# Kernel optimization log

Measured on AMD Instinct MI355X. Metric: run time of the kernel, lower is better.

Reference implementation:

```python
import jax, jax.numpy as jnp
import numpy as np

NUM_HEADS = 6
WS = 3

def setup_inputs() -> dict:
    key = jax.random.key(0)
    k1, k2, k3 = jax.random.split(key, 3)
    dim = 192
    x = jax.random.normal(k1, (2, dim, 48, 48, 48), dtype=jnp.float32)
    Wqkv = jax.random.normal(k2, (3 * dim, dim), dtype=jnp.float32) * (dim ** -0.5)
    Wproj = jax.random.normal(k3, (dim, dim), dtype=jnp.float32) * (dim ** -0.5)
    bproj = jnp.zeros((dim,), dtype=jnp.float32)
    return {"x": x, "Wqkv": Wqkv, "Wproj": Wproj, "bproj": bproj, "H": 384, "W": 288}

def reference(x, Wqkv, Wproj, bproj, H, W):
    b, c, h, w, d = x.shape
    xt = x.reshape(b, -1, c)                      # (B, N, C) with C = c, N = h*w*d
    B, N, C = xt.shape
    nh, ws = NUM_HEADS, WS
    hd = C // nh
    scale = hd ** -0.5
    hg, wg = H // ws, W // ws
    tg = hg * wg
    # window partition: (B, hg, ws, wg, ws, C) -> (B, hg, wg, ws, ws, C)
    xw = xt.reshape(B, hg, ws, wg, ws, C).transpose(0, 1, 3, 2, 4, 5)
    # fused QKV projection (no bias)
    qkv = jnp.einsum('bgvijc,oc->bgvijo', xw, Wqkv)          # (B,hg,wg,ws,ws,3C)
    qkv = qkv.reshape(B, tg, ws * ws, 3, nh, hd).transpose(3, 0, 1, 4, 2, 5)
    q, k, v = qkv[0], qkv[1], qkv[2]                          # (B, tg, nh, 9, hd)
    attn = jnp.einsum('bgnqd,bgnkd->bgnqk', q, k) * scale     # (B, tg, nh, 9, 9)
    attn = jax.nn.softmax(attn, axis=-1)
    out = jnp.einsum('bgnqk,bgnkd->bgnqd', attn, v)           # (B, tg, nh, 9, hd)
    out = out.transpose(0, 1, 3, 2, 4).reshape(B, hg, wg, ws, ws, C)
    out = jnp.swapaxes(out, 2, 3).reshape(B, N, C)            # un-window
    out = out @ Wproj.T + bproj
    return out.reshape(b, c, h, w, d)
```

## Files before the change

### kernel.cpp

```cpp
#include <hip/hip_runtime.h>

typedef _Float16 f16;
typedef _Float16 f16x4 __attribute__((ext_vector_type(4)));
typedef _Float16 f16x8 __attribute__((ext_vector_type(8)));
typedef float f32x4 __attribute__((ext_vector_type(4)));

#define TPB  576
#define NWIN 16
#define XS   200
#define WSS  200
#define QS   40
#define VS   264

#define WSQ_HALVES_PER_HEAD (96 * 200)
#define WSP_HALVES_PER_HEAD (192 * 40)
#define WS_NEEDED (230400 + 92160)

__device__ __forceinline__ void gload16(const void* g, void* l) {
    __builtin_amdgcn_global_load_lds(
        (const __attribute__((address_space(1))) unsigned int*)g,
        (__attribute__((address_space(3))) unsigned int*)l, 16, 0, 0);
}

__global__ __launch_bounds__(512) void conv_w(
    const float* __restrict__ Wqkv, const float* __restrict__ Wproj,
    f16* __restrict__ wsWq, f16* __restrict__ wsWp)
{
    int idx = blockIdx.x * 512 + threadIdx.x;
    if (idx < 110592) {
        int h = idx / (96 * 192), rem = idx % (96 * 192);
        int r = rem / 192, c = rem % 192;
        int grow = (r >> 5) * 192 + h * 32 + (r & 31);
        wsWq[(h * 96 + r) * 200 + c] = (f16)Wqkv[grow * 192 + c];
    } else {
        int j = idx - 110592;
        int h = j / (192 * 32), rem = j % (192 * 32);
        int r = rem / 32, c = rem % 32;
        wsWp[(h * 192 + r) * 40 + c] = (f16)Wproj[r * 192 + h * 32 + c];
    }
}

__global__ __launch_bounds__(TPB) void lsa_mfma10(
    const float* __restrict__ x, const f16* __restrict__ wsWq,
    const f16* __restrict__ wsWp, const float* __restrict__ bproj,
    float* __restrict__ out)
{
    __shared__ __attribute__((aligned(16))) f16 Xh[144 * XS];
    __shared__ __attribute__((aligned(16))) f16 Wh[96 * WSS];
    __shared__ __attribute__((aligned(16))) f16 Qh[144 * QS];
    __shared__ __attribute__((aligned(16))) f16 Kh[144 * QS];
    __shared__ __attribute__((aligned(16))) f16 Vt2[32 * VS];
    __shared__ __attribute__((aligned(16))) f16 AOh[144 * QS];
    __shared__ __attribute__((aligned(16))) f16 Wp[192 * QS];

    const int tid  = threadIdx.x;
    const int lane = tid & 63;
    const int w    = tid >> 6;
    const int ci   = w / 3;
    const int ti   = w % 3;
    const int l15  = lane & 15;
    const int lg   = lane >> 4;

    const int  bb    = blockIdx.x / 768;
    const int  gbase = (blockIdx.x % 768) * NWIN;
    const long rb0   = (long)bb * 110592 + (long)(gbase / 96) * 864 + (long)(gbase % 96) * 3;

    for (int l = tid; l < 2400; l += TPB)
        gload16(wsWq + l * 8, (char*)Wh + l * 16);
    for (int idx = tid; idx < 144 * 48; idx += TPB) {
        int t = idx / 48, c4 = idx % 48;
        int wi = t / 9, q = t - 9 * wi;
        long grow = rb0 + wi * 3 + (q / 3) * 288 + (q % 3);
        float4 xv = ((const float4*)x)[grow * 48 + c4];
        union { f16 h[4]; ushort4 u; } tmp;
        tmp.h[0] = (f16)xv.x; tmp.h[1] = (f16)xv.y; tmp.h[2] = (f16)xv.z; tmp.h[3] = (f16)xv.w;
        *(ushort4*)&Xh[t * XS + c4 * 4] = tmp.u;
    }
    {
        int4 z = {0, 0, 0, 0};
        for (int i2 = tid; i2 < (32 * VS * 2) / 16; i2 += TPB) ((int4*)Vt2)[i2] = z;
    }

    f32x4 pacc[3][4];
    #pragma unroll
    for (int a = 0; a < 3; ++a)
        #pragma unroll
        for (int bq = 0; bq < 4; ++bq)
            pacc[a][bq] = (f32x4){0.f, 0.f, 0.f, 0.f};

    __syncthreads();

    for (int h = 0; h < 6; ++h) {
        f32x4 qacc[2][3];
        #pragma unroll
        for (int c = 0; c < 2; ++c)
            #pragma unroll
            for (int t = 0; t < 3; ++t)
                qacc[c][t] = (f32x4){0.f, 0.f, 0.f, 0.f};
        #pragma unroll
        for (int kk = 0; kk < 6; ++kk) {
            f16x8 af[2], bf[3];
            #pragma unroll
            for (int c = 0; c < 2; ++c)
                af[c] = *(const f16x8*)&Wh[(16 * (ci + 3 * c) + l15) * WSS + kk * 32 + lg * 8];
            #pragma unroll
            for (int t = 0; t < 3; ++t)
                bf[t] = *(const f16x8*)&Xh[(16 * (ti + 3 * t) + l15) * XS + kk * 32 + lg * 8];
            #pragma unroll
            for (int c = 0; c < 2; ++c)
                #pragma unroll
                for (int t = 0; t < 3; ++t)
                    qacc[c][t] = __builtin_amdgcn_mfma_f32_16x16x32_f16(af[c], bf[t], qacc[c][t], 0, 0, 0);
        }
        #pragma unroll
        for (int c = 0; c < 2; ++c) {
            const int ct = ci + 3 * c;
            #pragma unroll
            for (int t = 0; t < 3; ++t) {
                const int token = 16 * (ti + 3 * t) + l15;
                f16x4 ph;
                ph[0] = (f16)qacc[c][t][0]; ph[1] = (f16)qacc[c][t][1];
                ph[2] = (f16)qacc[c][t][2]; ph[3] = (f16)qacc[c][t][3];
                if (ct < 2) {
                    *(f16x4*)&Qh[token * QS + ct * 16 + 4 * lg] = ph;
                } else if (ct < 4) {
                    *(f16x4*)&Kh[token * QS + (ct - 2) * 16 + 4 * lg] = ph;
                } else {
                    const int d0 = (ct - 4) * 16 + 4 * lg;
                    int wi = token / 9, qq = token - 9 * wi;
                    #pragma unroll
                    for (int r = 0; r < 4; ++r)
                        Vt2[(d0 + r) * VS + 16 * wi + qq] = ph[r];
                }
            }
        }
        __syncthreads();

        if (h < 5) {
            for (int l = tid; l < 2400; l += TPB)
                gload16(wsWq + (h + 1) * WSQ_HALVES_PER_HEAD + l * 8, (char*)Wh + l * 16);
        }
        for (int l = tid; l < 960; l += TPB)
            gload16(wsWp + h * WSP_HALVES_PER_HEAD + l * 8, (char*)Wp + l * 16);

        for (int wi = w; wi < NWIN; wi += 9) {
            int krow = 9 * wi + l15;
            krow = krow > 143 ? 143 : krow;
            f16x8 ak = *(const f16x8*)&Kh[krow * QS + lg * 8];
            f16x8 aq = *(const f16x8*)&Qh[krow * QS + lg * 8];
            f32x4 s = (f32x4){0.f, 0.f, 0.f, 0.f};
            s = __builtin_amdgcn_mfma_f32_16x16x32_f16(ak, aq, s, 0, 0, 0);
            float lgt[4];
            float mx = -1e30f;
            #pragma unroll
            for (int r = 0; r < 4; ++r) {
                int kx = 4 * lg + r;
                lgt[r] = (kx < 9) ? s[r] * 0.17677669529663687f : -1e30f;
                mx = fmaxf(mx, lgt[r]);
            }
            mx = fmaxf(mx, __shfl_xor(mx, 16));
            mx = fmaxf(mx, __shfl_xor(mx, 32));
            float e[4], sum = 0.f;
            #pragma unroll
            for (int r = 0; r < 4; ++r) {
                int kx = 4 * lg + r;
                e[r] = (kx < 9) ? __expf(lgt[r] - mx) : 0.f;
                sum += e[r];
            }
            sum += __shfl_xor(sum, 16);
            sum += __shfl_xor(sum, 32);
            float inv = 1.0f / sum;
            f16x4 p;
            p[0] = (f16)(e[0] * inv); p[1] = (f16)(e[1] * inv);
            p[2] = (f16)(e[2] * inv); p[3] = (f16)(e[3] * inv);
            #pragma unroll
            for (int dt = 0; dt < 2; ++dt) {
                f16x4 av = *(const f16x4*)&Vt2[(dt * 16 + l15) * VS + 16 * wi + 4 * lg];
                f32x4 o = (f32x4){0.f, 0.f, 0.f, 0.f};
                o = __builtin_amdgcn_mfma_f32_16x16x16f16(av, p, o, 0, 0, 0);
                if (l15 < 9) {
                    f16x4 oh;
                    oh[0] = (f16)o[0]; oh[1] = (f16)o[1]; oh[2] = (f16)o[2]; oh[3] = (f16)o[3];
                    *(f16x4*)&AOh[(9 * wi + l15) * QS + dt * 16 + 4 * lg] = oh;
                }
            }
        }
        __syncthreads();

        {
            f16x8 aof[3];
            #pragma unroll
            for (int a = 0; a < 3; ++a)
                aof[a] = *(const f16x8*)&AOh[(16 * (3 * ci + a) + l15) * QS + lg * 8];
            #pragma unroll
            for (int bq = 0; bq < 4; ++bq) {
                f16x8 bw = *(const f16x8*)&Wp[(16 * (4 * ti + bq) + l15) * QS + lg * 8];
                #pragma unroll
                for (int a = 0; a < 3; ++a)
                    pacc[a][bq] = __builtin_amdgcn_mfma_f32_16x16x32_f16(aof[a], bw, pacc[a][bq], 0, 0, 0);
            }
        }
    }

    float bv[4];
    #pragma unroll
    for (int bq = 0; bq < 4; ++bq)
        bv[bq] = bproj[16 * (4 * ti + bq) + l15];
    #pragma unroll
    for (int a = 0; a < 3; ++a) {
        #pragma unroll
        for (int r = 0; r < 4; ++r) {
            int t = 16 * (3 * ci + a) + lg * 4 + r;
            int wi = t / 9, q = t - 9 * wi;
            long grow = rb0 + wi * 3 + (q / 3) * 288 + (q % 3);
            float* dst = out + grow * 192;
            #pragma unroll
            for (int bq = 0; bq < 4; ++bq)
                dst[16 * (4 * ti + bq) + l15] = pacc[a][bq][r] + bv[bq];
        }
    }
}

__global__ __launch_bounds__(TPB) void lsa_mfma7(
    const float* __restrict__ x, const float* __restrict__ Wqkv,
    const float* __restrict__ Wproj, const float* __restrict__ bproj,
    float* __restrict__ out)
{
    __shared__ f16 Xh[144 * XS];
    __shared__ f16 Wh[96 * WSS];
    __shared__ f16 Qh[144 * QS];
    __shared__ f16 Kh[144 * QS];
    __shared__ f16 Vt2[32 * VS];
    __shared__ f16 AOh[144 * QS];
    __shared__ f16 Wp[192 * QS];

    const int tid  = threadIdx.x;
    const int lane = tid & 63;
    const int w    = tid >> 6;
    const int ci   = w / 3;
    const int ti   = w % 3;
    const int l15  = lane & 15;
    const int lg   = lane >> 4;

    const int  bb    = blockIdx.x / 768;
    const int  gbase = (blockIdx.x % 768) * NWIN;
    const long rb0   = (long)bb * 110592 + (long)(gbase / 96) * 864 + (long)(gbase % 96) * 3;

    const float4* Wq4 = (const float4*)Wqkv;
    const float4* Wp4 = (const float4*)Wproj;

    for (int idx = tid; idx < 144 * 48; idx += TPB) {
        int t = idx / 48, c4 = idx % 48;
        int wi = t / 9, q = t - 9 * wi;
        long grow = rb0 + wi * 3 + (q / 3) * 288 + (q % 3);
        float4 xv = ((const float4*)x)[grow * 48 + c4];
        union { f16 h[4]; ushort4 u; } tmp;
        tmp.h[0] = (f16)xv.x; tmp.h[1] = (f16)xv.y; tmp.h[2] = (f16)xv.z; tmp.h[3] = (f16)xv.w;
        *(ushort4*)&Xh[t * XS + c4 * 4] = tmp.u;
    }
    {
        int4 z = {0, 0, 0, 0};
        for (int i2 = tid; i2 < (32 * VS * 2) / 16; i2 += TPB) ((int4*)Vt2)[i2] = z;
    }
    #pragma unroll
    for (int i = 0; i < 8; ++i) {
        int l = i * TPB + tid;
        int r = l / 48, c4 = l % 48;
        float4 wv = Wq4[((r >> 5) * 192 + (r & 31)) * 48 + c4];
        union { f16 h4[4]; ushort4 u; } t;
        t.h4[0] = (f16)wv.x; t.h4[1] = (f16)wv.y; t.h4[2] = (f16)wv.z; t.h4[3] = (f16)wv.w;
        *(ushort4*)&Wh[r * WSS + c4 * 4] = t.u;
    }

    f32x4 pacc[3][4];
    #pragma unroll
    for (int a = 0; a < 3; ++a)
        #pragma unroll
        for (int bq = 0; bq < 4; ++bq)
            pacc[a][bq] = (f32x4){0.f, 0.f, 0.f, 0.f};

    __syncthreads();

    for (int h = 0; h < 6; ++h) {
        f32x4 qacc[2][3];
        #pragma unroll
        for (int c = 0; c < 2; ++c)
            #pragma unroll
            for (int t = 0; t < 3; ++t)
                qacc[c][t] = (f32x4){0.f, 0.f, 0.f, 0.f};
        #pragma unroll
        for (int kk = 0; kk < 6; ++kk) {
            f16x8 af[2], bf[3];
            #pragma unroll
            for (int c = 0; c < 2; ++c)
                af[c] = *(const f16x8*)&Wh[(16 * (ci + 3 * c) + l15) * WSS + kk * 32 + lg * 8];
            #pragma unroll
            for (int t = 0; t < 3; ++t)
                bf[t] = *(const f16x8*)&Xh[(16 * (ti + 3 * t) + l15) * XS + kk * 32 + lg * 8];
            #pragma unroll
            for (int c = 0; c < 2; ++c)
                #pragma unroll
                for (int t = 0; t < 3; ++t)
                    qacc[c][t] = __builtin_amdgcn_mfma_f32_16x16x32_f16(af[c], bf[t], qacc[c][t], 0, 0, 0);
        }
        #pragma unroll
        for (int c = 0; c < 2; ++c) {
            const int ct = ci + 3 * c;
            #pragma unroll
            for (int t = 0; t < 3; ++t) {
                const int token = 16 * (ti + 3 * t) + l15;
                f16x4 ph;
                ph[0] = (f16)qacc[c][t][0]; ph[1] = (f16)qacc[c][t][1];
                ph[2] = (f16)qacc[c][t][2]; ph[3] = (f16)qacc[c][t][3];
                if (ct < 2) {
                    *(f16x4*)&Qh[token * QS + ct * 16 + 4 * lg] = ph;
                } else if (ct < 4) {
                    *(f16x4*)&Kh[token * QS + (ct - 2) * 16 + 4 * lg] = ph;
                } else {
                    const int d0 = (ct - 4) * 16 + 4 * lg;
                    int wi = token / 9, qq = token - 9 * wi;
                    #pragma unroll
                    for (int r = 0; r < 4; ++r)
                        Vt2[(d0 + r) * VS + 16 * wi + qq] = ph[r];
                }
            }
        }
        __syncthreads();

        float4 wpv[3];
        if (tid < 512) {
            #pragma unroll
            for (int i = 0; i < 3; ++i) {
                int l = i * 512 + tid;
                int r = l / 8, c4 = l % 8;
                wpv[i] = Wp4[r * 48 + h * 8 + c4];
            }
        }
        if (h < 5) {
            #pragma unroll
            for (int i = 0; i < 8; ++i) {
                int l = i * TPB + tid;
                int r = l / 48, c4 = l % 48;
                float4 wv = Wq4[((r >> 5) * 192 + (h + 1) * 32 + (r & 31)) * 48 + c4];
                union { f16 h4[4]; ushort4 u; } t;
                t.h4[0] = (f16)wv.x; t.h4[1] = (f16)wv.y; t.h4[2] = (f16)wv.z; t.h4[3] = (f16)wv.w;
                *(ushort4*)&Wh[r * WSS + c4 * 4] = t.u;
            }
        }
        for (int wi = w; wi < NWIN; wi += 9) {
            int krow = 9 * wi + l15;
            krow = krow > 143 ? 143 : krow;
            f16x8 ak = *(const f16x8*)&Kh[krow * QS + lg * 8];
            f16x8 aq = *(const f16x8*)&Qh[krow * QS + lg * 8];
            f32x4 s = (f32x4){0.f, 0.f, 0.f, 0.f};
            s = __builtin_amdgcn_mfma_f32_16x16x32_f16(ak, aq, s, 0, 0, 0);
            float lgt[4];
            float mx = -1e30f;
            #pragma unroll
            for (int r = 0; r < 4; ++r) {
                int kx = 4 * lg + r;
                lgt[r] = (kx < 9) ? s[r] * 0.17677669529663687f : -1e30f;
                mx = fmaxf(mx, lgt[r]);
            }
            mx = fmaxf(mx, __shfl_xor(mx, 16));
            mx = fmaxf(mx, __shfl_xor(mx, 32));
            float e[4], sum = 0.f;
            #pragma unroll
            for (int r = 0; r < 4; ++r) {
                int kx = 4 * lg + r;
                e[r] = (kx < 9) ? __expf(lgt[r] - mx) : 0.f;
                sum += e[r];
            }
            sum += __shfl_xor(sum, 16);
            sum += __shfl_xor(sum, 32);
            float inv = 1.0f / sum;
            f16x4 p;
            p[0] = (f16)(e[0] * inv); p[1] = (f16)(e[1] * inv);
            p[2] = (f16)(e[2] * inv); p[3] = (f16)(e[3] * inv);
            #pragma unroll
            for (int dt = 0; dt < 2; ++dt) {
                f16x4 av = *(const f16x4*)&Vt2[(dt * 16 + l15) * VS + 16 * wi + 4 * lg];
                f32x4 o = (f32x4){0.f, 0.f, 0.f, 0.f};
                o = __builtin_amdgcn_mfma_f32_16x16x16f16(av, p, o, 0, 0, 0);
                if (l15 < 9) {
                    f16x4 oh;
                    oh[0] = (f16)o[0]; oh[1] = (f16)o[1]; oh[2] = (f16)o[2]; oh[3] = (f16)o[3];
                    *(f16x4*)&AOh[(9 * wi + l15) * QS + dt * 16 + 4 * lg] = oh;
                }
            }
        }
        if (tid < 512) {
            #pragma unroll
            for (int i = 0; i < 3; ++i) {
                int l = i * 512 + tid;
                int r = l / 8, c4 = l % 8;
                union { f16 h4[4]; ushort4 u; } t;
                t.h4[0] = (f16)wpv[i].x; t.h4[1] = (f16)wpv[i].y;
                t.h4[2] = (f16)wpv[i].z; t.h4[3] = (f16)wpv[i].w;
                *(ushort4*)&Wp[r * QS + c4 * 4] = t.u;
            }
        }
        __syncthreads();

        {
            f16x8 aof[3];
            #pragma unroll
            for (int a = 0; a < 3; ++a)
                aof[a] = *(const f16x8*)&AOh[(16 * (3 * ci + a) + l15) * QS + lg * 8];
            #pragma unroll
            for (int bq = 0; bq < 4; ++bq) {
                f16x8 bw = *(const f16x8*)&Wp[(16 * (4 * ti + bq) + l15) * QS + lg * 8];
                #pragma unroll
                for (int a = 0; a < 3; ++a)
                    pacc[a][bq] = __builtin_amdgcn_mfma_f32_16x16x32_f16(aof[a], bw, pacc[a][bq], 0, 0, 0);
            }
        }
    }

    float bv[4];
    #pragma unroll
    for (int bq = 0; bq < 4; ++bq)
        bv[bq] = bproj[16 * (4 * ti + bq) + l15];
    #pragma unroll
    for (int a = 0; a < 3; ++a) {
        #pragma unroll
        for (int r = 0; r < 4; ++r) {
            int t = 16 * (3 * ci + a) + lg * 4 + r;
            int wi = t / 9, q = t - 9 * wi;
            long grow = rb0 + wi * 3 + (q / 3) * 288 + (q % 3);
            float* dst = out + grow * 192;
            #pragma unroll
            for (int bq = 0; bq < 4; ++bq)
                dst[16 * (4 * ti + bq) + l15] = pacc[a][bq][r] + bv[bq];
        }
    }
}

extern "C" void kernel_launch(void* const* d_in, const int* in_sizes, int n_in,
                              void* d_out, int out_size, void* d_ws, size_t ws_size,
                              hipStream_t stream) {
    const float* x     = (const float*)d_in[0];
    const float* Wqkv  = (const float*)d_in[1];
    const float* Wproj = (const float*)d_in[2];
    const float* bproj = (const float*)d_in[3];
    float* out = (float*)d_out;
    if (ws_size >= (size_t)WS_NEEDED && d_ws != nullptr) {
        f16* wsWq = (f16*)d_ws;
        f16* wsWp = (f16*)((char*)d_ws + 230400);
        conv_w<<<288, 512, 0, stream>>>(Wqkv, Wproj, wsWq, wsWp);
        lsa_mfma10<<<1536, TPB, 0, stream>>>(x, wsWq, wsWp, bproj, out);
    } else {
        lsa_mfma7<<<1536, TPB, 0, stream>>>(x, Wqkv, Wproj, bproj, out);
    }
}
```

Baseline: 205.2 us.

## Pre-swizzle weights into MFMA fragment order and load them directly from global

```diff
diff --git a/kernel.cpp b/kernel.cpp
--- a/kernel.cpp
+++ b/kernel.cpp
@@ -12,46 +12,49 @@
 #define QS   40
 #define VS   264
 
-#define WSQ_HALVES_PER_HEAD (96 * 200)
-#define WSP_HALVES_PER_HEAD (192 * 40)
-#define WS_NEEDED (230400 + 92160)
-
-__device__ __forceinline__ void gload16(const void* g, void* l) {
-    __builtin_amdgcn_global_load_lds(
-        (const __attribute__((address_space(1))) unsigned int*)g,
-        (__attribute__((address_space(3))) unsigned int*)l, 16, 0, 0);
-}
+#define WSQF_HALVES 110592
+#define WS_NEEDED   (221184 + 73728)
 
 __global__ __launch_bounds__(512) void conv_w(
     const float* __restrict__ Wqkv, const float* __restrict__ Wproj,
-    f16* __restrict__ wsWq, f16* __restrict__ wsWp)
+    f16* __restrict__ wsWqf, f16* __restrict__ wsWpf)
 {
     int idx = blockIdx.x * 512 + threadIdx.x;
-    if (idx < 110592) {
-        int h = idx / (96 * 192), rem = idx % (96 * 192);
-        int r = rem / 192, c = rem % 192;
+    if (idx < WSQF_HALVES) {
+        int h    = idx / 18432;
+        int rem  = idx % 18432;
+        int ct   = rem / 3072;
+        int rem2 = rem % 3072;
+        int kk   = rem2 / 512;
+        int rem3 = rem2 % 512;
+        int lane = rem3 / 8;
+        int e    = rem3 % 8;
+        int r    = 16 * ct + (lane & 15);
         int grow = (r >> 5) * 192 + h * 32 + (r & 31);
-        wsWq[(h * 96 + r) * 200 + c] = (f16)Wqkv[grow * 192 + c];
+        int col  = kk * 32 + (lane >> 4) * 8 + e;
+        wsWqf[idx] = (f16)Wqkv[grow * 192 + col];
     } else {
-        int j = idx - 110592;
-        int h = j / (192 * 32), rem = j % (192 * 32);
-        int r = rem / 32, c = rem % 32;
-        wsWp[(h * 192 + r) * 40 + c] = (f16)Wproj[r * 192 + h * 32 + c];
+        int j    = idx - WSQF_HALVES;
+        int h    = j / 6144;
+        int rem  = j % 6144;
+        int nt   = rem / 512;
+        int rem2 = rem % 512;
+        int lane = rem2 / 8;
+        int e    = rem2 % 8;
+        wsWpf[j] = (f16)Wproj[(16 * nt + (lane & 15)) * 192 + h * 32 + (lane >> 4) * 8 + e];
     }
 }
 
-__global__ __launch_bounds__(TPB) void lsa_mfma10(
-    const float* __restrict__ x, const f16* __restrict__ wsWq,
-    const f16* __restrict__ wsWp, const float* __restrict__ bproj,
+__global__ __launch_bounds__(TPB) void lsa_mfma11(
+    const float* __restrict__ x, const f16* __restrict__ wsWqf,
+    const f16* __restrict__ wsWpf, const float* __restrict__ bproj,
     float* __restrict__ out)
 {
     __shared__ __attribute__((aligned(16))) f16 Xh[144 * XS];
-    __shared__ __attribute__((aligned(16))) f16 Wh[96 * WSS];
     __shared__ __attribute__((aligned(16))) f16 Qh[144 * QS];
     __shared__ __attribute__((aligned(16))) f16 Kh[144 * QS];
     __shared__ __attribute__((aligned(16))) f16 Vt2[32 * VS];
     __shared__ __attribute__((aligned(16))) f16 AOh[144 * QS];
-    __shared__ __attribute__((aligned(16))) f16 Wp[192 * QS];
 
     const int tid  = threadIdx.x;
     const int lane = tid & 63;
@@ -65,8 +68,9 @@
     const int  gbase = (blockIdx.x % 768) * NWIN;
     const long rb0   = (long)bb * 110592 + (long)(gbase / 96) * 864 + (long)(gbase % 96) * 3;
 
-    for (int l = tid; l < 2400; l += TPB)
-        gload16(wsWq + l * 8, (char*)Wh + l * 16);
+    const f16x8* wqf = (const f16x8*)wsWqf;
+    const f16x8* wpf = (const f16x8*)wsWpf;
+
     for (int idx = tid; idx < 144 * 48; idx += TPB) {
         int t = idx / 48, c4 = idx % 48;
         int wi = t / 9, q = t - 9 * wi;
@@ -100,9 +104,8 @@
         #pragma unroll
         for (int kk = 0; kk < 6; ++kk) {
             f16x8 af[2], bf[3];
-            #pragma unroll
-            for (int c = 0; c < 2; ++c)
-                af[c] = *(const f16x8*)&Wh[(16 * (ci + 3 * c) + l15) * WSS + kk * 32 + lg * 8];
+            af[0] = wqf[((h * 6 + ci    ) * 6 + kk) * 64 + lane];
+            af[1] = wqf[((h * 6 + ci + 3) * 6 + kk) * 64 + lane];
             #pragma unroll
             for (int t = 0; t < 3; ++t)
                 bf[t] = *(const f16x8*)&Xh[(16 * (ti + 3 * t) + l15) * XS + kk * 32 + lg * 8];
@@ -136,13 +139,6 @@
         }
         __syncthreads();
 
-        if (h < 5) {
-            for (int l = tid; l < 2400; l += TPB)
-                gload16(wsWq + (h + 1) * WSQ_HALVES_PER_HEAD + l * 8, (char*)Wh + l * 16);
-        }
-        for (int l = tid; l < 960; l += TPB)
-            gload16(wsWp + h * WSP_HALVES_PER_HEAD + l * 8, (char*)Wp + l * 16);
-
         for (int wi = w; wi < NWIN; wi += 9) {
             int krow = 9 * wi + l15;
             krow = krow > 143 ? 143 : krow;
@@ -188,17 +184,19 @@
         __syncthreads();
 
         {
+            f16x8 bw[4];
+            #pragma unroll
+            for (int bq = 0; bq < 4; ++bq)
+                bw[bq] = wpf[(h * 12 + 4 * ti + bq) * 64 + lane];
             f16x8 aof[3];
             #pragma unroll
             for (int a = 0; a < 3; ++a)
                 aof[a] = *(const f16x8*)&AOh[(16 * (3 * ci + a) + l15) * QS + lg * 8];
             #pragma unroll
-            for (int bq = 0; bq < 4; ++bq) {
-                f16x8 bw = *(const f16x8*)&Wp[(16 * (4 * ti + bq) + l15) * QS + lg * 8];
+            for (int bq = 0; bq < 4; ++bq)
                 #pragma unroll
                 for (int a = 0; a < 3; ++a)
-                    pacc[a][bq] = __builtin_amdgcn_mfma_f32_16x16x32_f16(aof[a], bw, pacc[a][bq], 0, 0, 0);
-            }
+                    pacc[a][bq] = __builtin_amdgcn_mfma_f32_16x16x32_f16(aof[a], bw[bq], pacc[a][bq], 0, 0, 0);
         }
     }
 
@@ -445,10 +443,10 @@
     const float* bproj = (const float*)d_in[3];
     float* out = (float*)d_out;
     if (ws_size >= (size_t)WS_NEEDED && d_ws != nullptr) {
-        f16* wsWq = (f16*)d_ws;
-        f16* wsWp = (f16*)((char*)d_ws + 230400);
-        conv_w<<<288, 512, 0, stream>>>(Wqkv, Wproj, wsWq, wsWp);
-        lsa_mfma10<<<1536, TPB, 0, stream>>>(x, wsWq, wsWp, bproj, out);
+        f16* wsWqf = (f16*)d_ws;
+        f16* wsWpf = (f16*)((char*)d_ws + 221184);
+        conv_w<<<288, 512, 0, stream>>>(Wqkv, Wproj, wsWqf, wsWpf);
+        lsa_mfma11<<<1536, TPB, 0, stream>>>(x, wsWqf, wsWpf, bproj, out);
     } else {
         lsa_mfma7<<<1536, TPB, 0, stream>>>(x, Wqkv, Wproj, bproj, out);
     }
```

Result: slower. 227.9 us (+11.0%).

## Use 12 waves per block and repartition QKV and projection MFMA work

Applied to the files above, without the earlier changes.

```diff
diff --git a/kernel.cpp b/kernel.cpp
--- a/kernel.cpp
+++ b/kernel.cpp
@@ -5,7 +5,8 @@
 typedef _Float16 f16x8 __attribute__((ext_vector_type(8)));
 typedef float f32x4 __attribute__((ext_vector_type(4)));
 
-#define TPB  576
+#define TPB  768
+#define TPBF 576
 #define NWIN 16
 #define XS   200
 #define WSS  200
@@ -40,7 +41,7 @@
     }
 }
 
-__global__ __launch_bounds__(TPB) void lsa_mfma10(
+__global__ __launch_bounds__(TPB) void lsa_mfma14(
     const float* __restrict__ x, const f16* __restrict__ wsWq,
     const f16* __restrict__ wsWp, const float* __restrict__ bproj,
     float* __restrict__ out)
@@ -56,8 +57,8 @@
     const int tid  = threadIdx.x;
     const int lane = tid & 63;
     const int w    = tid >> 6;
-    const int ci   = w / 3;
-    const int ti   = w % 3;
+    const int ci   = w % 3;
+    const int tg   = w / 3;
     const int l15  = lane & 15;
     const int lg   = lane >> 4;
 
@@ -67,7 +68,8 @@
 
     for (int l = tid; l < 2400; l += TPB)
         gload16(wsWq + l * 8, (char*)Wh + l * 16);
-    for (int idx = tid; idx < 144 * 48; idx += TPB) {
+    for (int i = 0; i < 9; ++i) {
+        int idx = i * TPB + tid;
         int t = idx / 48, c4 = idx % 48;
         int wi = t / 9, q = t - 9 * wi;
         long grow = rb0 + wi * 3 + (q / 3) * 288 + (q % 3);
@@ -79,6 +81,186 @@
     {
         int4 z = {0, 0, 0, 0};
         for (int i2 = tid; i2 < (32 * VS * 2) / 16; i2 += TPB) ((int4*)Vt2)[i2] = z;
+    }
+
+    f32x4 pacc[9];
+    #pragma unroll
+    for (int a = 0; a < 9; ++a) pacc[a] = (f32x4){0.f, 0.f, 0.f, 0.f};
+
+    __syncthreads();
+
+    for (int h = 0; h < 6; ++h) {
+        f32x4 qacc[2][3];
+        #pragma unroll
+        for (int c = 0; c < 2; ++c)
+            #pragma unroll
+            for (int t = 0; t < 3; ++t)
+                qacc[c][t] = (f32x4){0.f, 0.f, 0.f, 0.f};
+        #pragma unroll
+        for (int kk = 0; kk < 6; ++kk) {
+            f16x8 af[2];
+            af[0] = *(const f16x8*)&Wh[(16 * ci        + l15) * WSS + kk * 32 + lg * 8];
+            af[1] = *(const f16x8*)&Wh[(16 * (ci + 3)  + l15) * WSS + kk * 32 + lg * 8];
+            #pragma unroll
+            for (int t = 0; t < 3; ++t) {
+                int tt = tg + 4 * t;
+                if (tt < 9) {
+                    f16x8 bf = *(const f16x8*)&Xh[(16 * tt + l15) * XS + kk * 32 + lg * 8];
+                    qacc[0][t] = __builtin_amdgcn_mfma_f32_16x16x32_f16(af[0], bf, qacc[0][t], 0, 0, 0);
+                    qacc[1][t] = __builtin_amdgcn_mfma_f32_16x16x32_f16(af[1], bf, qacc[1][t], 0, 0, 0);
+                }
+            }
+        }
+        #pragma unroll
+        for (int c = 0; c < 2; ++c) {
+            const int ct = ci + 3 * c;
+            #pragma unroll
+            for (int t = 0; t < 3; ++t) {
+                int tt = tg + 4 * t;
+                if (tt < 9) {
+                    const int token = 16 * tt + l15;
+                    f16x4 ph;
+                    ph[0] = (f16)qacc[c][t][0]; ph[1] = (f16)qacc[c][t][1];
+                    ph[2] = (f16)qacc[c][t][2]; ph[3] = (f16)qacc[c][t][3];
+                    if (ct < 2) {
+                        *(f16x4*)&Qh[token * QS + ct * 16 + 4 * lg] = ph;
+                    } else if (ct < 4) {
+                        *(f16x4*)&Kh[token * QS + (ct - 2) * 16 + 4 * lg] = ph;
+                    } else {
+                        const int d0 = (ct - 4) * 16 + 4 * lg;
+                        int wi = token / 9, qq = token - 9 * wi;
+                        #pragma unroll
+                        for (int r = 0; r < 4; ++r)
+                            Vt2[(d0 + r) * VS + 16 * wi + qq] = ph[r];
+                    }
+                }
+            }
+        }
+        __syncthreads();
+
+        if (h < 5) {
+            for (int l = tid; l < 2400; l += TPB)
+                gload16(wsWq + (h + 1) * WSQ_HALVES_PER_HEAD + l * 8, (char*)Wh + l * 16);
+        }
+        for (int l = tid; l < 960; l += TPB)
+            gload16(wsWp + h * WSP_HALVES_PER_HEAD + l * 8, (char*)Wp + l * 16);
+
+        for (int wi = w; wi < NWIN; wi += 12) {
+            int krow = 9 * wi + l15;
+            krow = krow > 143 ? 143 : krow;
+            f16x8 ak = *(const f16x8*)&Kh[krow * QS + lg * 8];
+            f16x8 aq = *(const f16x8*)&Qh[krow * QS + lg * 8];
+            f32x4 s = (f32x4){0.f, 0.f, 0.f, 0.f};
+            s = __builtin_amdgcn_mfma_f32_16x16x32_f16(ak, aq, s, 0, 0, 0);
+            float lgt[4];
+            float mx = -1e30f;
+            #pragma unroll
+            for (int r = 0; r < 4; ++r) {
+                int kx = 4 * lg + r;
+                lgt[r] = (kx < 9) ? s[r] * 0.17677669529663687f : -1e30f;
+                mx = fmaxf(mx, lgt[r]);
+            }
+            mx = fmaxf(mx, __shfl_xor(mx, 16));
+            mx = fmaxf(mx, __shfl_xor(mx, 32));
+            float e[4], sum = 0.f;
+            #pragma unroll
+            for (int r = 0; r < 4; ++r) {
+                int kx = 4 * lg + r;
+                e[r] = (kx < 9) ? __expf(lgt[r] - mx) : 0.f;
+                sum += e[r];
+            }
+            sum += __shfl_xor(sum, 16);
+            sum += __shfl_xor(sum, 32);
+            float inv = 1.0f / sum;
+            f16x4 p;
+            p[0] = (f16)(e[0] * inv); p[1] = (f16)(e[1] * inv);
+            p[2] = (f16)(e[2] * inv); p[3] = (f16)(e[3] * inv);
+            #pragma unroll
+            for (int dt = 0; dt < 2; ++dt) {
+                f16x4 av = *(const f16x4*)&Vt2[(dt * 16 + l15) * VS + 16 * wi + 4 * lg];
+                f32x4 o = (f32x4){0.f, 0.f, 0.f, 0.f};
+                o = __builtin_amdgcn_mfma_f32_16x16x16f16(av, p, o, 0, 0, 0);
+                if (l15 < 9) {
+                    f16x4 oh;
+                    oh[0] = (f16)o[0]; oh[1] = (f16)o[1]; oh[2] = (f16)o[2]; oh[3] = (f16)o[3];
+                    *(f16x4*)&AOh[(9 * wi + l15) * QS + dt * 16 + 4 * lg] = oh;
+                }
+            }
+        }
+        __syncthreads();
+
+        {
+            f16x8 bw = *(const f16x8*)&Wp[(16 * w + l15) * QS + lg * 8];
+            #pragma unroll
+            for (int a = 0; a < 9; ++a) {
+                f16x8 aof = *(const f16x8*)&AOh[(16 * a + l15) * QS + lg * 8];
+                pacc[a] = __builtin_amdgcn_mfma_f32_16x16x32_f16(aof, bw, pacc[a], 0, 0, 0);
+            }
+        }
+    }
+
+    const float bv = bproj[16 * w + l15];
+    #pragma unroll
+    for (int a = 0; a < 9; ++a) {
+        #pragma unroll
+        for (int r = 0; r < 4; ++r) {
+            int t = 16 * a + lg * 4 + r;
+            int wi = t / 9, q = t - 9 * wi;
+            long grow = rb0 + wi * 3 + (q / 3) * 288 + (q % 3);
+            out[grow * 192 + 16 * w + l15] = pacc[a][r] + bv;
+        }
+    }
+}
+
+__global__ __launch_bounds__(TPBF) void lsa_mfma7(
+    const float* __restrict__ x, const float* __restrict__ Wqkv,
+    const float* __restrict__ Wproj, const float* __restrict__ bproj,
+    float* __restrict__ out)
+{
+    __shared__ f16 Xh[144 * XS];
+    __shared__ f16 Wh[96 * WSS];
+    __shared__ f16 Qh[144 * QS];
+    __shared__ f16 Kh[144 * QS];
+    __shared__ f16 Vt2[32 * VS];
+    __shared__ f16 AOh[144 * QS];
+    __shared__ f16 Wp[192 * QS];
+
+    const int tid  = threadIdx.x;
+    const int lane = tid & 63;
+    const int w    = tid >> 6;
+    const int ci   = w / 3;
+    const int ti   = w % 3;
+    const int l15  = lane & 15;
+    const int lg   = lane >> 4;
+
+    const int  bb    = blockIdx.x / 768;
+    const int  gbase = (blockIdx.x % 768) * NWIN;
+    const long rb0   = (long)bb * 110592 + (long)(gbase / 96) * 864 + (long)(gbase % 96) * 3;
+
+    const float4* Wq4 = (const float4*)Wqkv;
+    const float4* Wp4 = (const float4*)Wproj;
+
+    for (int idx = tid; idx < 144 * 48; idx += TPBF) {
+        int t = idx / 48, c4 = idx % 48;
+        int wi = t / 9, q = t - 9 * wi;
+        long grow = rb0 + wi * 3 + (q / 3) * 288 + (q % 3);
+        float4 xv = ((const float4*)x)[grow * 48 + c4];
+        union { f16 h[4]; ushort4 u; } tmp;
+        tmp.h[0] = (f16)xv.x; tmp.h[1] = (f16)xv.y; tmp.h[2] = (f16)xv.z; tmp.h[3] = (f16)xv.w;
+        *(ushort4*)&Xh[t * XS + c4 * 4] = tmp.u;
+    }
+    {
+        int4 z = {0, 0, 0, 0};
+        for (int i2 = tid; i2 < (32 * VS * 2) / 16; i2 += TPBF) ((int4*)Vt2)[i2] = z;
+    }
+    #pragma unroll
+    for (int i = 0; i < 8; ++i) {
+        int l = i * TPBF + tid;
+        int r = l / 48, c4 = l % 48;
+        float4 wv = Wq4[((r >> 5) * 192 + (r & 31)) * 48 + c4];
+        union { f16 h4[4]; ushort4 u; } t;
+        t.h4[0] = (f16)wv.x; t.h4[1] = (f16)wv.y; t.h4[2] = (f16)wv.z; t.h4[3] = (f16)wv.w;
+        *(ushort4*)&Wh[r * WSS + c4 * 4] = t.u;
     }
 
     f32x4 pacc[3][4];
@@ -136,197 +318,6 @@
         }
         __syncthreads();
 
-        if (h < 5) {
-            for (int l = tid; l < 2400; l += TPB)
-                gload16(wsWq + (h + 1) * WSQ_HALVES_PER_HEAD + l * 8, (char*)Wh + l * 16);
-        }
-        for (int l = tid; l < 960; l += TPB)
-            gload16(wsWp + h * WSP_HALVES_PER_HEAD + l * 8, (char*)Wp + l * 16);
-
-        for (int wi = w; wi < NWIN; wi += 9) {
-            int krow = 9 * wi + l15;
-            krow = krow > 143 ? 143 : krow;
-            f16x8 ak = *(const f16x8*)&Kh[krow * QS + lg * 8];
-            f16x8 aq = *(const f16x8*)&Qh[krow * QS + lg * 8];
-            f32x4 s = (f32x4){0.f, 0.f, 0.f, 0.f};
-            s = __builtin_amdgcn_mfma_f32_16x16x32_f16(ak, aq, s, 0, 0, 0);
-            float lgt[4];
-            float mx = -1e30f;
-            #pragma unroll
-            for (int r = 0; r < 4; ++r) {
-                int kx = 4 * lg + r;
-                lgt[r] = (kx < 9) ? s[r] * 0.17677669529663687f : -1e30f;
-                mx = fmaxf(mx, lgt[r]);
-            }
-            mx = fmaxf(mx, __shfl_xor(mx, 16));
-            mx = fmaxf(mx, __shfl_xor(mx, 32));
-            float e[4], sum = 0.f;
-            #pragma unroll
-            for (int r = 0; r < 4; ++r) {
-                int kx = 4 * lg + r;
-                e[r] = (kx < 9) ? __expf(lgt[r] - mx) : 0.f;
-                sum += e[r];
-            }
-            sum += __shfl_xor(sum, 16);
-            sum += __shfl_xor(sum, 32);
-            float inv = 1.0f / sum;
-            f16x4 p;
-            p[0] = (f16)(e[0] * inv); p[1] = (f16)(e[1] * inv);
-            p[2] = (f16)(e[2] * inv); p[3] = (f16)(e[3] * inv);
-            #pragma unroll
-            for (int dt = 0; dt < 2; ++dt) {
-                f16x4 av = *(const f16x4*)&Vt2[(dt * 16 + l15) * VS + 16 * wi + 4 * lg];
-                f32x4 o = (f32x4){0.f, 0.f, 0.f, 0.f};
-                o = __builtin_amdgcn_mfma_f32_16x16x16f16(av, p, o, 0, 0, 0);
-                if (l15 < 9) {
-                    f16x4 oh;
-                    oh[0] = (f16)o[0]; oh[1] = (f16)o[1]; oh[2] = (f16)o[2]; oh[3] = (f16)o[3];
-                    *(f16x4*)&AOh[(9 * wi + l15) * QS + dt * 16 + 4 * lg] = oh;
-                }
-            }
-        }
-        __syncthreads();
-
-        {
-            f16x8 aof[3];
-            #pragma unroll
-            for (int a = 0; a < 3; ++a)
-                aof[a] = *(const f16x8*)&AOh[(16 * (3 * ci + a) + l15) * QS + lg * 8];
-            #pragma unroll
-            for (int bq = 0; bq < 4; ++bq) {
-                f16x8 bw = *(const f16x8*)&Wp[(16 * (4 * ti + bq) + l15) * QS + lg * 8];
-                #pragma unroll
-                for (int a = 0; a < 3; ++a)
-                    pacc[a][bq] = __builtin_amdgcn_mfma_f32_16x16x32_f16(aof[a], bw, pacc[a][bq], 0, 0, 0);
-            }
-        }
-    }
-
-    float bv[4];
-    #pragma unroll
-    for (int bq = 0; bq < 4; ++bq)
-        bv[bq] = bproj[16 * (4 * ti + bq) + l15];
-    #pragma unroll
-    for (int a = 0; a < 3; ++a) {
-        #pragma unroll
-        for (int r = 0; r < 4; ++r) {
-            int t = 16 * (3 * ci + a) + lg * 4 + r;
-            int wi = t / 9, q = t - 9 * wi;
-            long grow = rb0 + wi * 3 + (q / 3) * 288 + (q % 3);
-            float* dst = out + grow * 192;
-            #pragma unroll
-            for (int bq = 0; bq < 4; ++bq)
-                dst[16 * (4 * ti + bq) + l15] = pacc[a][bq][r] + bv[bq];
-        }
-    }
-}
-
-__global__ __launch_bounds__(TPB) void lsa_mfma7(
-    const float* __restrict__ x, const float* __restrict__ Wqkv,
-    const float* __restrict__ Wproj, const float* __restrict__ bproj,
-    float* __restrict__ out)
-{
-    __shared__ f16 Xh[144 * XS];
-    __shared__ f16 Wh[96 * WSS];
-    __shared__ f16 Qh[144 * QS];
-    __shared__ f16 Kh[144 * QS];
-    __shared__ f16 Vt2[32 * VS];
-    __shared__ f16 AOh[144 * QS];
-    __shared__ f16 Wp[192 * QS];
-
-    const int tid  = threadIdx.x;
-    const int lane = tid & 63;
-    const int w    = tid >> 6;
-    const int ci   = w / 3;
-    const int ti   = w % 3;
-    const int l15  = lane & 15;
-    const int lg   = lane >> 4;
-
-    const int  bb    = blockIdx.x / 768;
-    const int  gbase = (blockIdx.x % 768) * NWIN;
-    const long rb0   = (long)bb * 110592 + (long)(gbase / 96) * 864 + (long)(gbase % 96) * 3;
-
-    const float4* Wq4 = (const float4*)Wqkv;
-    const float4* Wp4 = (const float4*)Wproj;
-
-    for (int idx = tid; idx < 144 * 48; idx += TPB) {
-        int t = idx / 48, c4 = idx % 48;
-        int wi = t / 9, q = t - 9 * wi;
-        long grow = rb0 + wi * 3 + (q / 3) * 288 + (q % 3);
-        float4 xv = ((const float4*)x)[grow * 48 + c4];
-        union { f16 h[4]; ushort4 u; } tmp;
-        tmp.h[0] = (f16)xv.x; tmp.h[1] = (f16)xv.y; tmp.h[2] = (f16)xv.z; tmp.h[3] = (f16)xv.w;
-        *(ushort4*)&Xh[t * XS + c4 * 4] = tmp.u;
-    }
-    {
-        int4 z = {0, 0, 0, 0};
-        for (int i2 = tid; i2 < (32 * VS * 2) / 16; i2 += TPB) ((int4*)Vt2)[i2] = z;
-    }
-    #pragma unroll
-    for (int i = 0; i < 8; ++i) {
-        int l = i * TPB + tid;
-        int r = l / 48, c4 = l % 48;
-        float4 wv = Wq4[((r >> 5) * 192 + (r & 31)) * 48 + c4];
-        union { f16 h4[4]; ushort4 u; } t;
-        t.h4[0] = (f16)wv.x; t.h4[1] = (f16)wv.y; t.h4[2] = (f16)wv.z; t.h4[3] = (f16)wv.w;
-        *(ushort4*)&Wh[r * WSS + c4 * 4] = t.u;
-    }
-
-    f32x4 pacc[3][4];
-    #pragma unroll
-    for (int a = 0; a < 3; ++a)
-        #pragma unroll
-        for (int bq = 0; bq < 4; ++bq)
-            pacc[a][bq] = (f32x4){0.f, 0.f, 0.f, 0.f};
-
-    __syncthreads();
-
-    for (int h = 0; h < 6; ++h) {
-        f32x4 qacc[2][3];
-        #pragma unroll
-        for (int c = 0; c < 2; ++c)
-            #pragma unroll
-            for (int t = 0; t < 3; ++t)
-                qacc[c][t] = (f32x4){0.f, 0.f, 0.f, 0.f};
-        #pragma unroll
-        for (int kk = 0; kk < 6; ++kk) {
-            f16x8 af[2], bf[3];
-            #pragma unroll
-            for (int c = 0; c < 2; ++c)
-                af[c] = *(const f16x8*)&Wh[(16 * (ci + 3 * c) + l15) * WSS + kk * 32 + lg * 8];
-            #pragma unroll
-            for (int t = 0; t < 3; ++t)
-                bf[t] = *(const f16x8*)&Xh[(16 * (ti + 3 * t) + l15) * XS + kk * 32 + lg * 8];
-            #pragma unroll
-            for (int c = 0; c < 2; ++c)
-                #pragma unroll
-                for (int t = 0; t < 3; ++t)
-                    qacc[c][t] = __builtin_amdgcn_mfma_f32_16x16x32_f16(af[c], bf[t], qacc[c][t], 0, 0, 0);
-        }
-        #pragma unroll
-        for (int c = 0; c < 2; ++c) {
-            const int ct = ci + 3 * c;
-            #pragma unroll
-            for (int t = 0; t < 3; ++t) {
-                const int token = 16 * (ti + 3 * t) + l15;
-                f16x4 ph;
-                ph[0] = (f16)qacc[c][t][0]; ph[1] = (f16)qacc[c][t][1];
-                ph[2] = (f16)qacc[c][t][2]; ph[3] = (f16)qacc[c][t][3];
-                if (ct < 2) {
-                    *(f16x4*)&Qh[token * QS + ct * 16 + 4 * lg] = ph;
-                } else if (ct < 4) {
-                    *(f16x4*)&Kh[token * QS + (ct - 2) * 16 + 4 * lg] = ph;
-                } else {
-                    const int d0 = (ct - 4) * 16 + 4 * lg;
-                    int wi = token / 9, qq = token - 9 * wi;
-                    #pragma unroll
-                    for (int r = 0; r < 4; ++r)
-                        Vt2[(d0 + r) * VS + 16 * wi + qq] = ph[r];
-                }
-            }
-        }
-        __syncthreads();
-
         float4 wpv[3];
         if (tid < 512) {
             #pragma unroll
@@ -339,7 +330,7 @@
         if (h < 5) {
             #pragma unroll
             for (int i = 0; i < 8; ++i) {
-                int l = i * TPB + tid;
+                int l = i * TPBF + tid;
                 int r = l / 48, c4 = l % 48;
                 float4 wv = Wq4[((r >> 5) * 192 + (h + 1) * 32 + (r & 31)) * 48 + c4];
                 union { f16 h4[4]; ushort4 u; } t;
@@ -448,8 +439,8 @@
         f16* wsWq = (f16*)d_ws;
         f16* wsWp = (f16*)((char*)d_ws + 230400);
         conv_w<<<288, 512, 0, stream>>>(Wqkv, Wproj, wsWq, wsWp);
-        lsa_mfma10<<<1536, TPB, 0, stream>>>(x, wsWq, wsWp, bproj, out);
+        lsa_mfma14<<<1536, TPB, 0, stream>>>(x, wsWq, wsWp, bproj, out);
     } else {
-        lsa_mfma7<<<1536, TPB, 0, stream>>>(x, Wqkv, Wproj, bproj, out);
+        lsa_mfma7<<<1536, TPBF, 0, stream>>>(x, Wqkv, Wproj, bproj, out);
     }
 }
```

Result: faster. 198.3 us, median of 2 (-3.4%).
